# Kernel tuning notes

Measured on AMD Instinct MI355X. Metric: run time of the kernel, lower is better.

## Reference

```python
import jax, jax.numpy as jnp
import numpy as np

N = 768          # number of proposals (graph nodes)
C = 1024         # box_head feature dim (in_feats)
HC = 256         # RelPN hidden_c
K = 20           # topk edges per node
GH = 256         # gcn_hidden
H1 = 4           # gat1 heads
IMG_H, IMG_W = 800.0, 800.0
NEG_SLOPE = 0.2  # PyG GATConv leaky_relu slope


def setup_inputs() -> dict:
    key = jax.random.key(0)
    ks = jax.random.split(key, 24)
    s = 0.02
    feats = jax.random.normal(ks[0], (N, C), jnp.float32)
    # valid boxes inside an 800x800 image
    cx = jax.random.uniform(ks[1], (N,), minval=100.0, maxval=700.0)
    cy = jax.random.uniform(ks[2], (N,), minval=100.0, maxval=700.0)
    w = jax.random.uniform(ks[3], (N,), minval=10.0, maxval=200.0)
    h = jax.random.uniform(ks[4], (N,), minval=10.0, maxval=200.0)
    boxes = jnp.stack([cx - 0.5 * w, cy - 0.5 * h, cx + 0.5 * w, cy + 0.5 * h], axis=1)
    rn = lambda k, sh: jax.random.normal(k, sh, jnp.float32) * s
    return {
        'feats': feats, 'boxes': boxes,
        # RelationProposalNetwork: fc1(2C+4 -> HC), fc2(HC -> 1)
        'W1': rn(ks[5], (2 * C + 4, HC)), 'b1': jnp.zeros((HC,), jnp.float32),
        'W2': rn(ks[6], (HC, 1)), 'b2': jnp.zeros((1,), jnp.float32),
        # GATConv(C+4 -> GH, heads=4)
        'g1W': rn(ks[7], (C + 4, H1 * GH)), 'g1as': rn(ks[8], (H1, GH)),
        'g1ad': rn(ks[9], (H1, GH)), 'g1b': jnp.zeros((H1 * GH,), jnp.float32),
        # GATConv(GH*4 -> 2, heads=1)
        'g2W': rn(ks[10], (H1 * GH, 2)), 'g2as': rn(ks[11], (1, 2)),
        'g2ad': rn(ks[12], (1, 2)), 'g2b': jnp.zeros((2,), jnp.float32),
        'rW1': rn(ks[13], (H1 * GH + 4, GH // 2)), 'rb1': jnp.zeros((GH // 2,), jnp.float32),
        'rW2': rn(ks[14], (GH // 2, 4)), 'rb2': jnp.zeros((4,), jnp.float32),
    }


def _gat(xin, W, a_src, a_dst, bias, heads, feat, nbr):
    """PyG-style GATConv (eval mode, self-loops already in nbr). nbr: [N, K+1] src ids per dst."""
    n = xin.shape[0]
    xp = (xin @ W).reshape(n, heads, feat)              # [N,H,F]
    asrc = jnp.einsum('nhf,hf->nh', xp, a_src)          # [N,H]
    adst = jnp.einsum('nhf,hf->nh', xp, a_dst)          # [N,H]
    logits = jax.nn.leaky_relu(asrc[nbr] + adst[:, None, :], NEG_SLOPE)  # [N,K+1,H]
    alpha = jax.nn.softmax(logits, axis=1)              # softmax over incoming edges per dst
    out = jnp.einsum('nkh,nkhf->nhf', alpha, xp[nbr])   # gather + weighted aggregate
    return out.reshape(n, heads * feat) + bias


def reference(feats, boxes, W1, b1, W2, b2, g1W, g1as, g1ad, g1b,
              g2W, g2as, g2ad, g2b, rW1, rb1, rW2, rb2):
    n = feats.shape[0]
    scale = jnp.array([IMG_W, IMG_H, IMG_W, IMG_H], jnp.float32)
    geom = boxes / scale                                 # _box_geom: normalized coords
    x = jnp.concatenate([feats, geom], axis=1)           # [N, C+4]

    # --- RelationProposalNetwork: fc1(cat[f_i, f_j, |b_i - b_j|]) decomposed ---
    Wa, Wb, Wg = W1[:C], W1[C:2 * C], W1[2 * C:]
    fa = feats @ Wa                                      # i-part  [N,HC]
    fb = feats @ Wb                                      # j-part  [N,HC]
    gdiff = jnp.abs(boxes[:, None, :] - boxes[None, :, :])          # [N,N,4]
    h = jax.nn.relu(fa[:, None, :] + fb[None, :, :]
                    + jnp.einsum('ijd,dh->ijh', gdiff, Wg) + b1)    # [N,N,HC]
    rel = jnp.einsum('ijh,h->ij', h, W2[:, 0]) + b2[0]              # [N,N]

    # --- top-k edges per destination node (exclude self), plus self-loops ---
    rel_masked = jnp.where(jnp.eye(n, dtype=bool), -1e9, rel)
    _, nbr = jax.lax.top_k(rel_masked, K)                # [N,K] src j for each dst i
    nbr = jnp.concatenate([nbr, jnp.arange(n)[:, None]], axis=1)    # [N,K+1]

    # --- GAT propagation ---
    h1 = jax.nn.relu(_gat(x, g1W, g1as, g1ad, g1b, H1, GH, nbr))    # [N,1024]
    logits = _gat(h1, g2W, g2as, g2ad, g2b, 1, 2, nbr)              # [N,2]

    reg_in = jnp.concatenate([h1, geom], axis=1)
    delta = jax.nn.relu(reg_in @ rW1 + rb1) @ rW2 + rb2             # [N,4]
    px0, py0, px1, py1 = boxes[:, 0], boxes[:, 1], boxes[:, 2], boxes[:, 3]
    pw, ph = px1 - px0, py1 - py0
    pcx, pcy = px0 + 0.5 * pw, py0 + 0.5 * ph
    dx, dy, dw, dh = delta[:, 0], delta[:, 1], delta[:, 2], delta[:, 3]
    gcx, gcy = dx * pw + pcx, dy * ph + pcy
    gw, gh = jnp.exp(dw) * pw, jnp.exp(dh) * ph
    final_boxes = jnp.stack([gcx - 0.5 * gw, gcy - 0.5 * gh,
                             gcx + 0.5 * gw, gcy + 0.5 * gh], axis=1)
    return jnp.concatenate([logits, final_boxes], axis=1)  # [N,6]
```

## Files before the change

### kernel.cpp

```cpp
#include <hip/hip_runtime.h>
#include <math.h>

#define NN 768
#define KK_TOP 20
#define NBR_K 21

typedef __attribute__((ext_vector_type(8))) short bf16x8;
typedef __attribute__((ext_vector_type(4))) float f32x4;
typedef unsigned short ushort_t;
typedef unsigned int uint_t;

__device__ __forceinline__ ushort_t f2bf(float x) {
    union { float f; uint_t u; } c; c.f = x;
    uint_t r = (c.u + 0x7FFFu + ((c.u >> 16) & 1u)) >> 16;
    return (ushort_t)r;
}
__device__ __forceinline__ float bf2f(ushort_t u) {
    union { uint_t u; float f; } c; c.u = ((uint_t)u) << 16;
    return c.f;
}

struct Params {
    const float *feats, *boxes, *W1, *b1, *W2, *b2;
    const float *g1W, *g1as, *g1ad, *g1b, *g2W, *g2as, *g2ad, *g2b;
    const float *rW1, *rb1, *rW2, *rb2;
    float *out;
    float *fafb, *xp, *relm, *hid, *Arow, *Brow, *asrc, *adst, *xp2, *aux2;
    float4 *wgt4; float *w2p, *consts;
    float *va, *vb, *av;
    int *nbr;
    ushort_t *featsbf, *btAB, *btG, *btR, *h1bf;
};

__global__ __launch_bounds__(256) void k_prep(Params P)
{
    int b = blockIdx.x, t = threadIdx.x;
    if (b == 800) {
        const float* Wg = P.W1 + 2048 * 256;
        float q0 = Wg[t], q1 = Wg[256 + t], q2 = Wg[512 + t], q3 = Wg[768 + t];
        float w2 = P.W2[t];
        P.wgt4[t] = make_float4(q0, q1, q2, q3);
        P.w2p[t] = w2;
        __shared__ float red[256];
        float vals[5] = {q0 * w2, q1 * w2, q2 * w2, q3 * w2, P.b1[t] * w2};
        for (int d = 0; d < 5; d++) {
            red[t] = vals[d]; __syncthreads();
            for (int s = 128; s > 0; s >>= 1) {
                if (t < s) red[t] += red[t + s];
                __syncthreads();
            }
            if (t == 0) P.consts[d] = red[0];
            __syncthreads();
        }
        return;
    }
    if (b >= 809) {
        int o = (b - 809) * 256 + t;
        if (o >= 8224) return;
        int vec = o / 1028, k = o - vec * 1028;
        int h = vec & 3;
        const float* aw = ((vec < 4) ? P.g1as : P.g1ad) + h * 256;
        const float* gw = P.g1W + (size_t)k * 1024 + h * 256;
        float s = 0.f;
        for (int f = 0; f < 256; f++) s += gw[f] * aw[f];
        P.av[vec * 1028 + k] = s;
        return;
    }
    if (b >= 801) {
        int o = (b - 801) * 256 + t;
        const float* row = P.W1 + (size_t)o * 256;
        float s = 0.f;
        for (int h = 0; h < 256; h++) s += row[h] * P.W2[h];
        if (o < 1024) P.va[o] = s; else P.vb[o - 1024] = s;
        return;
    }
    if (b >= 416) {
        int gid = (b - 416) * 2048 + t * 8;
        float4 v0 = *(const float4*)(P.feats + gid);
        float4 v1 = *(const float4*)(P.feats + gid + 4);
        uint4 r;
        r.x = (uint_t)f2bf(v0.x) | ((uint_t)f2bf(v0.y) << 16);
        r.y = (uint_t)f2bf(v0.z) | ((uint_t)f2bf(v0.w) << 16);
        r.z = (uint_t)f2bf(v1.x) | ((uint_t)f2bf(v1.y) << 16);
        r.w = (uint_t)f2bf(v1.z) | ((uint_t)f2bf(v1.w) << 16);
        *(uint4*)(P.featsbf + gid) = r;
        return;
    }
    const float* in; ushort_t* out; int ldN, tk, tn;
    if (b < 64)       { in = P.W1;              out = P.btAB;              ldN = 256;  tn = b & 3;  tk = b >> 2; }
    else if (b < 128) { int i = b - 64;  in = P.W1 + 1024 * 256; out = P.btAB + 256 * 1024; ldN = 256;  tn = i & 3;  tk = i >> 2; }
    else if (b < 384) { int i = b - 128; in = P.g1W;             out = P.btG;               ldN = 1024; tn = i & 15; tk = i >> 4; }
    else              { int i = b - 384; in = P.rW1;             out = P.btR;               ldN = 128;  tn = i & 1;  tk = i >> 1; }

    __shared__ __align__(16) float tile[64][68];
    int k0 = tk * 64, n0 = tn * 64;
#pragma unroll
    for (int it = 0; it < 4; it++) {
        int r = (t >> 4) + it * 16;
        int c = (t & 15) * 4;
        *(float4*)&tile[r][c] = *(const float4*)(in + (size_t)(k0 + r) * ldN + n0 + c);
    }
    __syncthreads();
    int n = t >> 2;
    int kc = (t & 3) * 16;
    uint_t p[8];
#pragma unroll
    for (int h = 0; h < 8; h++) {
        ushort_t lo = f2bf(tile[kc + 2 * h][n]);
        ushort_t hi = f2bf(tile[kc + 2 * h + 1][n]);
        p[h] = (uint_t)lo | ((uint_t)hi << 16);
    }
    ushort_t* dst = out + (size_t)(n0 + n) * 1024 + k0 + kc;
    *(uint4*)dst = make_uint4(p[0], p[1], p[2], p[3]);
    *(uint4*)(dst + 8) = make_uint4(p[4], p[5], p[6], p[7]);
}

__device__ __forceinline__ void mfma_unit(
    int bx, int by, const ushort_t* __restrict__ A, const ushort_t* __restrict__ Bt,
    float* __restrict__ C, int ldc, int mode,
    const float* __restrict__ boxes, const float* __restrict__ Wgeo,
    const float* __restrict__ bias, int t, char* smem)
{
    ushort_t (*As)[72] = (ushort_t(*)[72])smem;
    ushort_t (*Bs)[72] = (ushort_t(*)[72])(smem + 64 * 72 * 2);
    int m0 = by * 64, n0 = bx * 64;
    int lane = t & 63, w = t >> 6;
    int quad = lane >> 4, ci = lane & 15;

    int r0 = t >> 3, q0 = t & 7;
    int r1 = (t + 256) >> 3, q1 = (t + 256) & 7;

    const ushort_t* Abase = A + (size_t)(m0 + r0) * 1024 + q0 * 8;
    const ushort_t* Abase1 = A + (size_t)(m0 + r1) * 1024 + q1 * 8;
    const ushort_t* Bbase = Bt + (size_t)(n0 + r0) * 1024 + q0 * 8;
    const ushort_t* Bbase1 = Bt + (size_t)(n0 + r1) * 1024 + q1 * 8;

    uint4 pa0 = *(const uint4*)(Abase);
    uint4 pa1 = *(const uint4*)(Abase1);
    uint4 pb0 = *(const uint4*)(Bbase);
    uint4 pb1 = *(const uint4*)(Bbase1);

    f32x4 acc[2][2];
    acc[0][0] = (f32x4){0.f, 0.f, 0.f, 0.f};
    acc[0][1] = (f32x4){0.f, 0.f, 0.f, 0.f};
    acc[1][0] = (f32x4){0.f, 0.f, 0.f, 0.f};
    acc[1][1] = (f32x4){0.f, 0.f, 0.f, 0.f};

    int arow = (w & 1) * 32 + ci;
    int brow = (w >> 1) * 32 + ci;

    for (int kt = 0; kt < 16; kt++) {
        *(uint4*)&As[r0][q0 * 8] = pa0;
        *(uint4*)&As[r1][q1 * 8] = pa1;
        *(uint4*)&Bs[r0][q0 * 8] = pb0;
        *(uint4*)&Bs[r1][q1 * 8] = pb1;
        __syncthreads();
        if (kt < 15) {
            int ko = (kt + 1) * 64;
            pa0 = *(const uint4*)(Abase + ko);
            pa1 = *(const uint4*)(Abase1 + ko);
            pb0 = *(const uint4*)(Bbase + ko);
            pb1 = *(const uint4*)(Bbase1 + ko);
        }
#pragma unroll
        for (int s = 0; s < 2; s++) {
            int kb = s * 32 + quad * 8;
            bf16x8 a0 = *(const bf16x8*)&As[arow][kb];
            bf16x8 a1 = *(const bf16x8*)&As[arow + 16][kb];
            bf16x8 b0 = *(const bf16x8*)&Bs[brow][kb];
            bf16x8 b1 = *(const bf16x8*)&Bs[brow + 16][kb];
            acc[0][0] = __builtin_amdgcn_mfma_f32_16x16x32_bf16(a0, b0, acc[0][0], 0, 0, 0);
            acc[0][1] = __builtin_amdgcn_mfma_f32_16x16x32_bf16(a0, b1, acc[0][1], 0, 0, 0);
            acc[1][0] = __builtin_amdgcn_mfma_f32_16x16x32_bf16(a1, b0, acc[1][0], 0, 0, 0);
            acc[1][1] = __builtin_amdgcn_mfma_f32_16x16x32_bf16(a1, b1, acc[1][1], 0, 0, 0);
        }
        __syncthreads();
    }

    const float inv800 = 1.0f / 800.0f;
#pragma unroll
    for (int ni = 0; ni < 2; ni++) {
        int col = n0 + (w >> 1) * 32 + ni * 16 + ci;
        float wg0 = 0.f, wg1 = 0.f, wg2 = 0.f, wg3 = 0.f, bv = 0.f;
        if (mode) {
            wg0 = Wgeo[col]; wg1 = Wgeo[ldc + col];
            wg2 = Wgeo[2 * ldc + col]; wg3 = Wgeo[3 * ldc + col];
            if (mode == 2) bv = bias[col];
        }
#pragma unroll
        for (int mi = 0; mi < 2; mi++) {
            int rbase = m0 + (w & 1) * 32 + mi * 16 + quad * 4;
#pragma unroll
            for (int reg = 0; reg < 4; reg++) {
                int row = rbase + reg;
                float v = acc[mi][ni][reg];
                if (mode) {
                    float4 bx4 = *(const float4*)(boxes + row * 4);
                    v += (bx4.x * wg0 + bx4.y * wg1 + bx4.z * wg2 + bx4.w * wg3) * inv800 + bv;
                    if (mode == 2) v = fmaxf(v, 0.f);
                }
                C[(size_t)row * ldc + col] = v;
            }
        }
    }
}

__global__ __launch_bounds__(256) void k_gemms(Params P)
{
    __shared__ __align__(16) char smem[18432];
    int u = blockIdx.x, t = threadIdx.x;
    if (u < 96) {
        mfma_unit(u & 7, u >> 3, P.featsbf, P.btAB, P.fafb, 512, 0,
                  nullptr, nullptr, nullptr, t, smem);
    } else if (u < 288) {
        int v = u - 96;
        mfma_unit(v & 15, v >> 4, P.featsbf, P.btG, P.xp, 1024, 1,
                  P.boxes, P.g1W + (size_t)1024 * 1024, nullptr, t, smem);
    } else if (u < 480) {
        int row = (u - 288) * 4 + (t >> 6);
        int lane = t & 63;
        const float4* fr = (const float4*)(P.feats + (size_t)row * 1024);
        const float4* va4 = (const float4*)P.va;
        const float4* vb4 = (const float4*)P.vb;
        float s1 = 0.f, s2 = 0.f;
#pragma unroll
        for (int it = 0; it < 4; it++) {
            int idx = it * 64 + lane;
            float4 f = fr[idx], a = va4[idx], b = vb4[idx];
            s1 += f.x * a.x + f.y * a.y + f.z * a.z + f.w * a.w;
            s2 += f.x * b.x + f.y * b.y + f.z * b.z + f.w * b.w;
        }
#pragma unroll
        for (int off = 32; off > 0; off >>= 1) {
            s1 += __shfl_xor(s1, off);
            s2 += __shfl_xor(s2, off);
        }
        if (lane == 0) { P.Arow[row] = s1; P.Brow[row] = s2; }
    } else {
        int pair = (u - 480) * 4 + (t >> 6);
        int lane = t & 63;
        int n = pair >> 2, h = pair & 3;
        const float4* fr = (const float4*)(P.feats + (size_t)n * 1024);
        const float* vs = P.av + h * 1028;
        const float* vd = P.av + (4 + h) * 1028;
        const float4* vs4 = (const float4*)vs;
        const float4* vd4 = (const float4*)vd;
        float s1 = 0.f, s2 = 0.f;
#pragma unroll
        for (int it = 0; it < 4; it++) {
            int idx = it * 64 + lane;
            float4 f = fr[idx], a = vs4[idx], b = vd4[idx];
            s1 += f.x * a.x + f.y * a.y + f.z * a.z + f.w * a.w;
            s2 += f.x * b.x + f.y * b.y + f.z * b.z + f.w * b.w;
        }
#pragma unroll
        for (int off = 32; off > 0; off >>= 1) {
            s1 += __shfl_xor(s1, off);
            s2 += __shfl_xor(s2, off);
        }
        if (lane == 0) {
            const float inv800 = 1.0f / 800.0f;
            float4 bx = *(const float4*)(P.boxes + n * 4);
            float g0 = bx.x * inv800, g1 = bx.y * inv800, g2 = bx.z * inv800, g3 = bx.w * inv800;
            s1 += g0 * vs[1024] + g1 * vs[1025] + g2 * vs[1026] + g3 * vs[1027];
            s2 += g0 * vd[1024] + g1 * vd[1025] + g2 * vd[1026] + g3 * vd[1027];
            P.asrc[n * 4 + h] = s1;
            P.adst[n * 4 + h] = s2;
        }
    }
}

#define REL_ACC(FA0, FA1, FB0, FB1, Q, W)                                           \
    {                                                                               \
        float v;                                                                    \
        v = FA0 + FB0;                                                              \
        v = fmaf(g00.x, Q.x, v); v = fmaf(g00.y, Q.y, v);                           \
        v = fmaf(g00.z, Q.z, v); v = fmaf(g00.w, Q.w, v);                           \
        acc00 = fmaf(fabsf(v), W, acc00);                                           \
        v = FA0 + FB1;                                                              \
        v = fmaf(g01.x, Q.x, v); v = fmaf(g01.y, Q.y, v);                           \
        v = fmaf(g01.z, Q.z, v); v = fmaf(g01.w, Q.w, v);                           \
        acc01 = fmaf(fabsf(v), W, acc01);                                           \
        v = FA1 + FB0;                                                              \
        v = fmaf(g10.x, Q.x, v); v = fmaf(g10.y, Q.y, v);                           \
        v = fmaf(g10.z, Q.z, v); v = fmaf(g10.w, Q.w, v);                           \
        acc10 = fmaf(fabsf(v), W, acc10);                                           \
        v = FA1 + FB1;                                                              \
        v = fmaf(g11.x, Q.x, v); v = fmaf(g11.y, Q.y, v);                           \
        v = fmaf(g11.z, Q.z, v); v = fmaf(g11.w, Q.w, v);                           \
        acc11 = fmaf(fabsf(v), W, acc11);                                           \
    }

__global__ __launch_bounds__(256) void k_rel(Params P)
{
    __shared__ __align__(16) float fas[32][68];
    __shared__ __align__(16) float fbs[32][68];
    int t = threadIdx.x;
    int bx = blockIdx.x % 24, by = blockIdx.x / 24;
    int tx = t & 15, ty = t >> 4;
    int i0 = by * 32, j0 = bx * 32;
    int ia = i0 + ty, ib = i0 + ty + 16;
    int ja = j0 + tx, jb = j0 + tx + 16;

    float4 Bi0 = *(const float4*)(P.boxes + ia * 4);
    float4 Bi1 = *(const float4*)(P.boxes + ib * 4);
    float4 Bj0 = *(const float4*)(P.boxes + ja * 4);
    float4 Bj1 = *(const float4*)(P.boxes + jb * 4);
    float4 g00 = make_float4(fabsf(Bi0.x - Bj0.x), fabsf(Bi0.y - Bj0.y), fabsf(Bi0.z - Bj0.z), fabsf(Bi0.w - Bj0.w));
    float4 g01 = make_float4(fabsf(Bi0.x - Bj1.x), fabsf(Bi0.y - Bj1.y), fabsf(Bi0.z - Bj1.z), fabsf(Bi0.w - Bj1.w));
    float4 g10 = make_float4(fabsf(Bi1.x - Bj0.x), fabsf(Bi1.y - Bj0.y), fabsf(Bi1.z - Bj0.z), fabsf(Bi1.w - Bj0.w));
    float4 g11 = make_float4(fabsf(Bi1.x - Bj1.x), fabsf(Bi1.y - Bj1.y), fabsf(Bi1.z - Bj1.z), fabsf(Bi1.w - Bj1.w));

    float acc00 = 0.f, acc01 = 0.f, acc10 = 0.f, acc11 = 0.f;

    for (int p = 0; p < 4; p++) {
        for (int e = t; e < 512; e += 256) {
            int r = e >> 4, cq = e & 15;
            float4 bb = *(const float4*)(P.b1 + p * 64 + cq * 4);
            float4 fv = *(const float4*)(P.fafb + (size_t)(i0 + r) * 512 + p * 64 + cq * 4);
            float4 gv = *(const float4*)(P.fafb + (size_t)(j0 + r) * 512 + 256 + p * 64 + cq * 4);
            *(float4*)&fas[r][cq * 4] = make_float4(fv.x + bb.x, fv.y + bb.y, fv.z + bb.z, fv.w + bb.w);
            *(float4*)&fbs[r][cq * 4] = gv;
        }
        __syncthreads();
        const float4* wg = P.wgt4 + p * 64;
        const float* w2 = P.w2p + p * 64;
#pragma unroll 8
        for (int hc = 0; hc < 16; hc++) {
            int h4 = hc * 4;
            float4 fa0 = *(const float4*)&fas[ty][h4];
            float4 fa1 = *(const float4*)&fas[ty + 16][h4];
            float4 fb0 = *(const float4*)&fbs[tx][h4];
            float4 fb1 = *(const float4*)&fbs[tx + 16][h4];
            float4 w2v = *(const float4*)(w2 + h4);
            float4 q0 = wg[h4], q1 = wg[h4 + 1], q2 = wg[h4 + 2], q3 = wg[h4 + 3];
            REL_ACC(fa0.x, fa1.x, fb0.x, fb1.x, q0, w2v.x);
            REL_ACC(fa0.y, fa1.y, fb0.y, fb1.y, q1, w2v.y);
            REL_ACC(fa0.z, fa1.z, fb0.z, fb1.z, q2, w2v.z);
            REL_ACC(fa0.w, fa1.w, fb0.w, fb1.w, q3, w2v.w);
        }
        __syncthreads();
    }

    float c0 = P.consts[0], c1 = P.consts[1], c2 = P.consts[2], c3 = P.consts[3], c4 = P.consts[4];
    float b2v = P.b2[0];
    float Ai0 = P.Arow[ia], Ai1 = P.Arow[ib];
    float Bja = P.Brow[ja], Bjb = P.Brow[jb];

    float lin, r00, r01, r10, r11;
    lin = Ai0 + Bja + g00.x * c0 + g00.y * c1 + g00.z * c2 + g00.w * c3 + c4;
    r00 = 0.5f * (lin + acc00) + b2v;
    lin = Ai0 + Bjb + g01.x * c0 + g01.y * c1 + g01.z * c2 + g01.w * c3 + c4;
    r01 = 0.5f * (lin + acc01) + b2v;
    lin = Ai1 + Bja + g10.x * c0 + g10.y * c1 + g10.z * c2 + g10.w * c3 + c4;
    r10 = 0.5f * (lin + acc10) + b2v;
    lin = Ai1 + Bjb + g11.x * c0 + g11.y * c1 + g11.z * c2 + g11.w * c3 + c4;
    r11 = 0.5f * (lin + acc11) + b2v;
    P.relm[(size_t)ia * NN + ja] = (ia == ja) ? -1e9f : r00;
    P.relm[(size_t)ia * NN + jb] = (ia == jb) ? -1e9f : r01;
    P.relm[(size_t)ib * NN + ja] = (ib == ja) ? -1e9f : r10;
    P.relm[(size_t)ib * NN + jb] = (ib == jb) ? -1e9f : r11;
}

__global__ __launch_bounds__(256) void k_topkgat1(Params P)
{
    int n = blockIdx.x, t = threadIdx.x;
    __shared__ int nb[NBR_K];
    __shared__ float alpha[NBR_K][4];

    if (t < 64) {
        int lane = t;
        const float* rp = P.relm + (size_t)n * NN;
        float v[12];
#pragma unroll
        for (int q = 0; q < 12; q++) v[q] = rp[q * 64 + lane];
        for (int kk = 0; kk < KK_TOP; kk++) {
            float best = v[0]; int bq = 0;
#pragma unroll
            for (int q = 1; q < 12; q++) {
                if (v[q] > best) { best = v[q]; bq = q; }
            }
            int bidx = bq * 64 + lane;
#pragma unroll
            for (int off = 32; off > 0; off >>= 1) {
                float ov = __shfl_xor(best, off);
                int oi = __shfl_xor(bidx, off);
                if (ov > best || (ov == best && oi < bidx)) { best = ov; bidx = oi; }
            }
            if (lane == 0) { nb[kk] = bidx; P.nbr[n * NBR_K + kk] = bidx; }
            int bl = bidx & 63, bq2 = bidx >> 6;
            if (lane == bl) {
#pragma unroll
                for (int q = 0; q < 12; q++)
                    if (q == bq2) v[q] = -INFINITY;
            }
        }
        if (lane == 0) { nb[KK_TOP] = n; P.nbr[n * NBR_K + KK_TOP] = n; }
    }
    __syncthreads();

    if (t < NBR_K * 4) {
        int k = t % NBR_K, h = t / NBR_K;
        float e = P.asrc[nb[k] * 4 + h] + P.adst[n * 4 + h];
        e = (e > 0.f) ? e : 0.2f * e;
        alpha[k][h] = e;
    }
    __syncthreads();
    if (t < 4) {
        float m = -INFINITY;
        for (int k = 0; k < NBR_K; k++) m = fmaxf(m, alpha[k][t]);
        float s = 0.f;
        for (int k = 0; k < NBR_K; k++) { float ex = expf(alpha[k][t] - m); alpha[k][t] = ex; s += ex; }
        float inv = 1.f / s;
        for (int k = 0; k < NBR_K; k++) alpha[k][t] *= inv;
    }
    __syncthreads();
#pragma unroll
    for (int q = 0; q < 4; q++) {
        int c = q * 256 + t;
        int h = c >> 8;
        float acc = 0.f;
        for (int k = 0; k < NBR_K; k++) acc += alpha[k][h] * P.xp[(size_t)nb[k] * 1024 + c];
        P.h1bf[(size_t)n * 1024 + c] = f2bf(fmaxf(acc + P.g1b[c], 0.f));
    }
}

__global__ __launch_bounds__(256) void k_p6(Params P)
{
    __shared__ __align__(16) char smem[18432];
    int u = blockIdx.x, t = threadIdx.x;
    if (u < 192) {
        int wid = u * 4 + (t >> 6);
        int lane = t & 63;
        float s0 = 0.f, s1 = 0.f;
#pragma unroll
        for (int it = 0; it < 4; it++) {
            int k = it * 256 + lane * 4;
            uint2 pk = *(const uint2*)(P.h1bf + (size_t)wid * 1024 + k);
            float v0 = bf2f((ushort_t)(pk.x & 0xFFFF));
            float v1 = bf2f((ushort_t)(pk.x >> 16));
            float v2 = bf2f((ushort_t)(pk.y & 0xFFFF));
            float v3 = bf2f((ushort_t)(pk.y >> 16));
            float4 w0 = *(const float4*)(P.g2W + k * 2);
            float4 w1 = *(const float4*)(P.g2W + k * 2 + 4);
            s0 += v0 * w0.x + v1 * w0.z + v2 * w1.x + v3 * w1.z;
            s1 += v0 * w0.y + v1 * w0.w + v2 * w1.y + v3 * w1.w;
        }
#pragma unroll
        for (int off = 32; off > 0; off >>= 1) { s0 += __shfl_down(s0, off); s1 += __shfl_down(s1, off); }
        if (lane == 0) {
            P.xp2[wid * 2 + 0] = s0; P.xp2[wid * 2 + 1] = s1;
            P.aux2[wid * 2 + 0] = s0 * P.g2as[0] + s1 * P.g2as[1];
            P.aux2[wid * 2 + 1] = s0 * P.g2ad[0] + s1 * P.g2ad[1];
        }
    } else {
        int v = u - 192;
        mfma_unit(v & 1, v >> 1, P.h1bf, P.btR, P.hid, 128, 2,
                  P.boxes, P.rW1 + (size_t)1024 * 128, P.rb1, t, smem);
    }
}

__global__ __launch_bounds__(256) void k_p7(Params P)
{
    int u = blockIdx.x, t = threadIdx.x;
    if (u < 3) {
        int n = u * 256 + t;
        float adstv = P.aux2[n * 2 + 1];
        int nb[NBR_K];
        float e[NBR_K];
        float m = -INFINITY;
        for (int k = 0; k < NBR_K; k++) {
            nb[k] = P.nbr[n * NBR_K + k];
            float v = P.aux2[nb[k] * 2 + 0] + adstv;
            v = (v > 0.f) ? v : 0.2f * v;
            e[k] = v; m = fmaxf(m, v);
        }
        float s = 0.f;
        for (int k = 0; k < NBR_K; k++) { e[k] = expf(e[k] - m); s += e[k]; }
        float inv = 1.f / s;
        float o0 = 0.f, o1 = 0.f;
        for (int k = 0; k < NBR_K; k++) {
            float a = e[k] * inv;
            o0 += a * P.xp2[nb[k] * 2 + 0];
            o1 += a * P.xp2[nb[k] * 2 + 1];
        }
        P.out[n * 6 + 0] = o0 + P.g2b[0];
        P.out[n * 6 + 1] = o1 + P.g2b[1];
    } else {
        int n = (u - 3) * 256 + t;
        float d0 = 0.f, d1 = 0.f, d2 = 0.f, d3 = 0.f;
        for (int k = 0; k < 128; k++) {
            float v = P.hid[n * 128 + k];
            d0 += v * P.rW2[k * 4 + 0];
            d1 += v * P.rW2[k * 4 + 1];
            d2 += v * P.rW2[k * 4 + 2];
            d3 += v * P.rW2[k * 4 + 3];
        }
        d0 += P.rb2[0]; d1 += P.rb2[1]; d2 += P.rb2[2]; d3 += P.rb2[3];
        float x0 = P.boxes[n * 4 + 0], y0 = P.boxes[n * 4 + 1];
        float x1 = P.boxes[n * 4 + 2], y1 = P.boxes[n * 4 + 3];
        float pw = x1 - x0, ph = y1 - y0;
        float pcx = x0 + 0.5f * pw, pcy = y0 + 0.5f * ph;
        float gcx = d0 * pw + pcx, gcy = d1 * ph + pcy;
        float gw = expf(d2) * pw, gh = expf(d3) * ph;
        P.out[n * 6 + 2] = gcx - 0.5f * gw;
        P.out[n * 6 + 3] = gcy - 0.5f * gh;
        P.out[n * 6 + 4] = gcx + 0.5f * gw;
        P.out[n * 6 + 5] = gcy + 0.5f * gh;
    }
}

extern "C" void kernel_launch(void* const* d_in, const int* in_sizes, int n_in,
                              void* d_out, int out_size, void* d_ws, size_t ws_size,
                              hipStream_t stream)
{
    Params P;
    P.feats = (const float*)d_in[0];
    P.boxes = (const float*)d_in[1];
    P.W1    = (const float*)d_in[2];
    P.b1    = (const float*)d_in[3];
    P.W2    = (const float*)d_in[4];
    P.b2    = (const float*)d_in[5];
    P.g1W   = (const float*)d_in[6];
    P.g1as  = (const float*)d_in[7];
    P.g1ad  = (const float*)d_in[8];
    P.g1b   = (const float*)d_in[9];
    P.g2W   = (const float*)d_in[10];
    P.g2as  = (const float*)d_in[11];
    P.g2ad  = (const float*)d_in[12];
    P.g2b   = (const float*)d_in[13];
    P.rW1   = (const float*)d_in[14];
    P.rb1   = (const float*)d_in[15];
    P.rW2   = (const float*)d_in[16];
    P.rb2   = (const float*)d_in[17];
    P.out   = (float*)d_out;

    float* ws = (float*)d_ws;
    P.fafb  = ws;
    P.xp    = P.fafb + 393216;
    P.relm  = P.xp + 786432;
    P.hid   = P.relm + 589824;
    P.Arow  = P.hid + 98304;
    P.Brow  = P.Arow + 768;
    P.asrc  = P.Brow + 768;
    P.adst  = P.asrc + 3072;
    P.xp2   = P.adst + 3072;
    P.aux2  = P.xp2 + 1536;
    P.wgt4  = (float4*)(P.aux2 + 1536);
    P.w2p   = (float*)(P.wgt4 + 256);
    P.consts= P.w2p + 256;
    P.va    = P.consts + 8;
    P.vb    = P.va + 1024;
    P.av    = P.vb + 1024;
    P.nbr   = (int*)(P.av + 8224);
    P.featsbf = (ushort_t*)(P.nbr + 16128);
    P.btAB    = P.featsbf + 786432;
    P.btG     = P.btAB + 524288;
    P.btR     = P.btG + 1048576;
    P.h1bf    = P.btR + 131072;

    k_prep    <<<dim3(842),  dim3(256), 0, stream>>>(P);
    k_gemms   <<<dim3(1248), dim3(256), 0, stream>>>(P);
    k_rel     <<<dim3(576),  dim3(256), 0, stream>>>(P);
    k_topkgat1<<<dim3(768),  dim3(256), 0, stream>>>(P);
    k_p6      <<<dim3(216),  dim3(256), 0, stream>>>(P);
    k_p7      <<<dim3(6),    dim3(256), 0, stream>>>(P);
}
```

Measured before the change: 207.3 us.

## Parallelize weight-vector dot products and GAT2 softmax with wave reductions

The precompute dot products (W1·W2 rows and g1W·attention vectors) move from one thread per output with a serial 256-long loop to one wavefront per output, using float4 loads and shuffle reductions. The prep grid grows to fit this. The GAT2 edge softmax in k_p7 now uses one wave per node with lane-parallel neighbours instead of one thread per node. The GAT1 aggregation uses float4 gathers with packed bf16 stores, and the regressor's second layer caches rW2 in shared memory and reads hid with float4 loads. Together these cut serial latency and uncoalesced access in small, low-occupancy stages, at the cost of more blocks and more shuffle work.

```diff
diff --git a/kernel.cpp b/kernel.cpp
--- a/kernel.cpp
+++ b/kernel.cpp
@@ -54,24 +54,31 @@
         }
         return;
     }
-    if (b >= 809) {
-        int o = (b - 809) * 256 + t;
+    if (b >= 1313) {
+        int o = (b - 1313) * 4 + (t >> 6);
+        int lane = t & 63;
         if (o >= 8224) return;
         int vec = o / 1028, k = o - vec * 1028;
         int h = vec & 3;
-        const float* aw = ((vec < 4) ? P.g1as : P.g1ad) + h * 256;
-        const float* gw = P.g1W + (size_t)k * 1024 + h * 256;
-        float s = 0.f;
-        for (int f = 0; f < 256; f++) s += gw[f] * aw[f];
-        P.av[vec * 1028 + k] = s;
+        const float4* aw = (const float4*)(((vec < 4) ? P.g1as : P.g1ad) + h * 256);
+        const float4* gw = (const float4*)(P.g1W + (size_t)k * 1024 + h * 256);
+        float4 a = aw[lane], g = gw[lane];
+        float s = a.x * g.x + a.y * g.y + a.z * g.z + a.w * g.w;
+#pragma unroll
+        for (int off = 32; off > 0; off >>= 1) s += __shfl_xor(s, off);
+        if (lane == 0) P.av[o] = s;
         return;
     }
     if (b >= 801) {
-        int o = (b - 801) * 256 + t;
-        const float* row = P.W1 + (size_t)o * 256;
-        float s = 0.f;
-        for (int h = 0; h < 256; h++) s += row[h] * P.W2[h];
-        if (o < 1024) P.va[o] = s; else P.vb[o - 1024] = s;
+        int o = (b - 801) * 4 + (t >> 6);
+        int lane = t & 63;
+        const float4* row = (const float4*)(P.W1 + (size_t)o * 256);
+        float4 w = ((const float4*)P.W2)[lane];
+        float4 f = row[lane];
+        float s = f.x * w.x + f.y * w.y + f.z * w.z + f.w * w.w;
+#pragma unroll
+        for (int off = 32; off > 0; off >>= 1) s += __shfl_xor(s, off);
+        if (lane == 0) { if (o < 1024) P.va[o] = s; else P.vb[o - 1024] = s; }
         return;
     }
     if (b >= 416) {
@@ -415,14 +422,21 @@
         for (int k = 0; k < NBR_K; k++) alpha[k][t] *= inv;
     }
     __syncthreads();
-#pragma unroll
-    for (int q = 0; q < 4; q++) {
-        int c = q * 256 + t;
-        int h = c >> 8;
-        float acc = 0.f;
-        for (int k = 0; k < NBR_K; k++) acc += alpha[k][h] * P.xp[(size_t)nb[k] * 1024 + c];
-        P.h1bf[(size_t)n * 1024 + c] = f2bf(fmaxf(acc + P.g1b[c], 0.f));
-    }
+
+    int h = t >> 6;
+    float ax = 0.f, ay = 0.f, az = 0.f, aw = 0.f;
+#pragma unroll 7
+    for (int k = 0; k < NBR_K; k++) {
+        float a = alpha[k][h];
+        float4 xv = ((const float4*)(P.xp + (size_t)nb[k] * 1024))[t];
+        ax = fmaf(a, xv.x, ax); ay = fmaf(a, xv.y, ay);
+        az = fmaf(a, xv.z, az); aw = fmaf(a, xv.w, aw);
+    }
+    float4 gb = ((const float4*)P.g1b)[t];
+    uint2 pk;
+    pk.x = (uint_t)f2bf(fmaxf(ax + gb.x, 0.f)) | ((uint_t)f2bf(fmaxf(ay + gb.y, 0.f)) << 16);
+    pk.y = (uint_t)f2bf(fmaxf(az + gb.z, 0.f)) | ((uint_t)f2bf(fmaxf(aw + gb.w, 0.f)) << 16);
+    *(uint2*)(P.h1bf + (size_t)n * 1024 + t * 4) = pk;
 }
 
 __global__ __launch_bounds__(256) void k_p6(Params P)
@@ -462,52 +476,66 @@
 
 __global__ __launch_bounds__(256) void k_p7(Params P)
 {
+    __shared__ __align__(16) float rw2s[512];
     int u = blockIdx.x, t = threadIdx.x;
-    if (u < 3) {
-        int n = u * 256 + t;
+    if (u < 192) {
+        int n = u * 4 + (t >> 6);
+        int lane = t & 63;
         float adstv = P.aux2[n * 2 + 1];
-        int nb[NBR_K];
-        float e[NBR_K];
-        float m = -INFINITY;
-        for (int k = 0; k < NBR_K; k++) {
-            nb[k] = P.nbr[n * NBR_K + k];
-            float v = P.aux2[nb[k] * 2 + 0] + adstv;
-            v = (v > 0.f) ? v : 0.2f * v;
-            e[k] = v; m = fmaxf(m, v);
-        }
-        float s = 0.f;
-        for (int k = 0; k < NBR_K; k++) { e[k] = expf(e[k] - m); s += e[k]; }
-        float inv = 1.f / s;
-        float o0 = 0.f, o1 = 0.f;
-        for (int k = 0; k < NBR_K; k++) {
-            float a = e[k] * inv;
-            o0 += a * P.xp2[nb[k] * 2 + 0];
-            o1 += a * P.xp2[nb[k] * 2 + 1];
-        }
-        P.out[n * 6 + 0] = o0 + P.g2b[0];
-        P.out[n * 6 + 1] = o1 + P.g2b[1];
-    } else {
-        int n = (u - 3) * 256 + t;
-        float d0 = 0.f, d1 = 0.f, d2 = 0.f, d3 = 0.f;
-        for (int k = 0; k < 128; k++) {
-            float v = P.hid[n * 128 + k];
-            d0 += v * P.rW2[k * 4 + 0];
-            d1 += v * P.rW2[k * 4 + 1];
-            d2 += v * P.rW2[k * 4 + 2];
-            d3 += v * P.rW2[k * 4 + 3];
-        }
-        d0 += P.rb2[0]; d1 += P.rb2[1]; d2 += P.rb2[2]; d3 += P.rb2[3];
-        float x0 = P.boxes[n * 4 + 0], y0 = P.boxes[n * 4 + 1];
-        float x1 = P.boxes[n * 4 + 2], y1 = P.boxes[n * 4 + 3];
-        float pw = x1 - x0, ph = y1 - y0;
-        float pcx = x0 + 0.5f * pw, pcy = y0 + 0.5f * ph;
-        float gcx = d0 * pw + pcx, gcy = d1 * ph + pcy;
-        float gw = expf(d2) * pw, gh = expf(d3) * ph;
-        P.out[n * 6 + 2] = gcx - 0.5f * gw;
-        P.out[n * 6 + 3] = gcy - 0.5f * gh;
-        P.out[n * 6 + 4] = gcx + 0.5f * gw;
-        P.out[n * 6 + 5] = gcy + 0.5f * gh;
-    }
+        float e = -INFINITY, x0 = 0.f, x1 = 0.f;
+        if (lane < NBR_K) {
+            int nbk = P.nbr[n * NBR_K + lane];
+            float vv = P.aux2[nbk * 2 + 0] + adstv;
+            e = (vv > 0.f) ? vv : 0.2f * vv;
+            x0 = P.xp2[nbk * 2 + 0];
+            x1 = P.xp2[nbk * 2 + 1];
+        }
+        float m = e;
+#pragma unroll
+        for (int off = 32; off > 0; off >>= 1) m = fmaxf(m, __shfl_xor(m, off));
+        float ex = (lane < NBR_K) ? expf(e - m) : 0.f;
+        float ssum = ex, o0 = ex * x0, o1 = ex * x1;
+#pragma unroll
+        for (int off = 32; off > 0; off >>= 1) {
+            ssum += __shfl_xor(ssum, off);
+            o0 += __shfl_xor(o0, off);
+            o1 += __shfl_xor(o1, off);
+        }
+        if (lane == 0) {
+            float inv = 1.f / ssum;
+            P.out[n * 6 + 0] = o0 * inv + P.g2b[0];
+            P.out[n * 6 + 1] = o1 * inv + P.g2b[1];
+        }
+        return;
+    }
+    *(float2*)&rw2s[t * 2] = *(const float2*)(P.rW2 + t * 2);
+    __syncthreads();
+    int n = (u - 192) * 256 + t;
+    const float4* hrow = (const float4*)(P.hid + (size_t)n * 128);
+    float d0 = 0.f, d1 = 0.f, d2 = 0.f, d3 = 0.f;
+#pragma unroll 8
+    for (int k4 = 0; k4 < 32; k4++) {
+        float4 h = hrow[k4];
+        const float* wv = &rw2s[k4 * 16];
+        d0 = fmaf(h.x, wv[0], d0);  d1 = fmaf(h.x, wv[1], d1);
+        d2 = fmaf(h.x, wv[2], d2);  d3 = fmaf(h.x, wv[3], d3);
+        d0 = fmaf(h.y, wv[4], d0);  d1 = fmaf(h.y, wv[5], d1);
+        d2 = fmaf(h.y, wv[6], d2);  d3 = fmaf(h.y, wv[7], d3);
+        d0 = fmaf(h.z, wv[8], d0);  d1 = fmaf(h.z, wv[9], d1);
+        d2 = fmaf(h.z, wv[10], d2); d3 = fmaf(h.z, wv[11], d3);
+        d0 = fmaf(h.w, wv[12], d0); d1 = fmaf(h.w, wv[13], d1);
+        d2 = fmaf(h.w, wv[14], d2); d3 = fmaf(h.w, wv[15], d3);
+    }
+    d0 += P.rb2[0]; d1 += P.rb2[1]; d2 += P.rb2[2]; d3 += P.rb2[3];
+    float4 bx = *(const float4*)(P.boxes + n * 4);
+    float pw = bx.z - bx.x, ph = bx.w - bx.y;
+    float pcx = bx.x + 0.5f * pw, pcy = bx.y + 0.5f * ph;
+    float gcx = d0 * pw + pcx, gcy = d1 * ph + pcy;
+    float gw = expf(d2) * pw, gh = expf(d3) * ph;
+    P.out[n * 6 + 2] = gcx - 0.5f * gw;
+    P.out[n * 6 + 3] = gcy - 0.5f * gh;
+    P.out[n * 6 + 4] = gcx + 0.5f * gw;
+    P.out[n * 6 + 5] = gcy + 0.5f * gh;
 }
 
 extern "C" void kernel_launch(void* const* d_in, const int* in_sizes, int n_in,
@@ -559,10 +587,10 @@
     P.btR     = P.btG + 1048576;
     P.h1bf    = P.btR + 131072;
 
-    k_prep    <<<dim3(842),  dim3(256), 0, stream>>>(P);
+    k_prep    <<<dim3(3369), dim3(256), 0, stream>>>(P);
     k_gemms   <<<dim3(1248), dim3(256), 0, stream>>>(P);
     k_rel     <<<dim3(576),  dim3(256), 0, stream>>>(P);
     k_topkgat1<<<dim3(768),  dim3(256), 0, stream>>>(P);
     k_p6      <<<dim3(216),  dim3(256), 0, stream>>>(P);
-    k_p7      <<<dim3(6),    dim3(256), 0, stream>>>(P);
-}
+    k_p7      <<<dim3(195),  dim3(256), 0, stream>>>(P);
+}
```

After: 184.1 us. 1.13x faster.
